# Performance work log

Measured on AMD Instinct MI355X. Metric: run time of the kernel, lower is better.

The kernel has to match this reference:

```python
import jax, jax.numpy as jnp
import numpy as np

NUM_CLASSES = 80
PRE_NMS_K = 400    # pre_nms_points / max_output_size_per_class
MAX_BOXES = 200    # max_total_size
NMS_THRESH = 0.6
SCORE_THRESH = 0.0  # iou_thresh in YoloLayer, used as score threshold/mask
SCALE_XY = (1.2, 1.1, 1.05)  # levels 3,4,5
STRIDES = (8.0, 16.0, 32.0)  # 2**level


def setup_inputs() -> dict:
    key = jax.random.key(0)
    k3, k4, k5 = jax.random.split(key, 3)
    B, C5 = 8, 3 * (NUM_CLASSES + 5)
    p3 = jax.random.normal(k3, (B, 64, 64, C5), dtype=jnp.float32)
    p4 = jax.random.normal(k4, (B, 32, 32, C5), dtype=jnp.float32)
    p5 = jax.random.normal(k5, (B, 16, 16, C5), dtype=jnp.float32)
    a3 = jnp.array([[12., 16.], [19., 36.], [40., 28.]], jnp.float32)
    a4 = jnp.array([[36., 75.], [76., 55.], [72., 146.]], jnp.float32)
    a5 = jnp.array([[142., 110.], [192., 243.], [459., 401.]], jnp.float32)
    return {"p3": p3, "p4": p4, "p5": p5, "a3": a3, "a4": a4, "a5": a5}


def _decode_level(p, anchors, stride, scale_xy):
    # p: [B,H,W,A*(C+5)] raw head output; 'original' box decode (sigmoid xy, exp wh)
    B, H, W, _ = p.shape
    A = anchors.shape[0]
    d = p.reshape(B, H, W, A, NUM_CLASSES + 5)
    txy, twh, tobj, tcls = d[..., :2], d[..., 2:4], d[..., 4:5], d[..., 5:]
    gx, gy = jnp.meshgrid(jnp.arange(W, dtype=p.dtype), jnp.arange(H, dtype=p.dtype))
    grid = jnp.stack([gx, gy], -1)[None, :, :, None, :]          # [1,H,W,1,2] (x,y)
    sxy = jnp.asarray(scale_xy, p.dtype)
    xy = (jax.nn.sigmoid(txy) * sxy - 0.5 * (sxy - 1.0) + grid) / jnp.array([W, H], p.dtype)
    wh = jnp.exp(twh) * anchors[None, None, None] / jnp.array([W * stride, H * stride], p.dtype)
    x1y1 = xy - 0.5 * wh
    x2y2 = xy + 0.5 * wh
    boxes = jnp.stack([x1y1[..., 1], x1y1[..., 0], x2y2[..., 1], x2y2[..., 0]], -1)  # yxyx
    obj = jax.nn.sigmoid(tobj)
    cls = jax.nn.sigmoid(tcls) * obj
    N = H * W * A
    return boxes.reshape(B, N, 4), cls.reshape(B, N, NUM_CLASSES), obj.reshape(B, N)


def _pairwise_iou(b):
    # b: [K,4] yxyx in [0,1]
    area = (b[:, 2] - b[:, 0]) * (b[:, 3] - b[:, 1])
    tl = jnp.maximum(b[:, None, :2], b[None, :, :2])
    br = jnp.minimum(b[:, None, 2:], b[None, :, 2:])
    wh = jnp.maximum(br - tl, 0.0)
    inter = wh[..., 0] * wh[..., 1]
    union = area[:, None] + area[None, :] - inter
    return inter / jnp.maximum(union, 1e-9)


def _greedy_nms_scores(boxes, scores):
    # boxes/scores already sorted by score descending; returns scores with suppressed -> 0
    K = scores.shape[0]
    overlap = _pairwise_iou(boxes) > NMS_THRESH
    idx = jnp.arange(K)

    def body(i, keep):
        sup = overlap[i] & (idx > i) & keep[i]
        return keep & ~sup

    keep = jax.lax.fori_loop(0, K, body, jnp.ones((K,), bool))
    return jnp.where(keep & (scores > SCORE_THRESH), scores, 0.0)


def _detections_per_image(boxes, cls_scores):
    # boxes [N,4], cls_scores [N,C] -> combined per-class NMS, top MAX_BOXES overall
    boxes = jnp.clip(boxes, 0.0, 1.0)  # combined NMS clips boxes by default

    def per_class(scores_c):
        vals, idx = jax.lax.top_k(scores_c, PRE_NMS_K)
        b = boxes[idx]
        return _greedy_nms_scores(b, vals), b

    kept_scores, kept_boxes = jax.vmap(per_class)(cls_scores.T)  # [C,K], [C,K,4]
    flat_s = kept_scores.reshape(-1)
    flat_b = kept_boxes.reshape(-1, 4)
    cls_ids = jnp.repeat(jnp.arange(NUM_CLASSES), PRE_NMS_K)
    top_s, top_i = jax.lax.top_k(flat_s, MAX_BOXES)
    top_b = flat_b[top_i]
    top_c = cls_ids[top_i].astype(jnp.float32)
    valid = top_s > 0.0
    top_b = jnp.where(valid[:, None], top_b, 0.0)
    top_c = jnp.where(valid, top_c, 0.0)
    num = jnp.sum(valid.astype(jnp.int32))
    return top_b, top_s, top_c, num


def _forward(p3, p4, p5, a3, a4, a5):
    boxes, cls_scores, obj_scores = [], [], []
    for (p, a), stride, sxy in zip(((p3, a3), (p4, a4), (p5, a5)), STRIDES, SCALE_XY):
        b, c, o = _decode_level(p, a, stride, sxy)
        boxes.append(b); cls_scores.append(c); obj_scores.append(o)
    boxes = jnp.concatenate(boxes, 1)            # [B,N,4]
    cls_scores = jnp.concatenate(cls_scores, 1)  # [B,N,C]
    obj_scores = jnp.concatenate(obj_scores, 1)  # [B,N]
    obj_mask = (obj_scores > SCORE_THRESH).astype(boxes.dtype)
    cls_mask = (cls_scores > SCORE_THRESH).astype(boxes.dtype)
    cls_scores = cls_scores * obj_mask[..., None] * cls_mask
    return jax.vmap(_detections_per_image)(boxes, cls_scores)


def reference(p3, p4, p5, a3, a4, a5):
    bbox, confidence, classes, num_detections = _forward(p3, p4, p5, a3, a4, a5)
    return bbox, confidence, classes, num_detections
```

## Files before the change

### kernel.cpp

```cpp
#include <hip/hip_runtime.h>
#include <math.h>

#define NCLS 80
#define PRE_K 400
#define MAX_BOXES 200
#define KEEP_CAP 200
#define N_TOT 16128
#define M_FIN (NCLS * KEEP_CAP)
#define NMS_T 0.6f
#define NTHR 512
#define CAP 512

typedef unsigned long long u64;
typedef unsigned int u32;
typedef unsigned short u16;

__device__ __forceinline__ float sigf(float x) { return 1.0f / (1.0f + expf(-x)); }

__device__ __forceinline__ float score_f32(int idx, int b, int c,
    const float* __restrict__ p3, const float* __restrict__ p4, const float* __restrict__ p5)
{
    const float* base; int W, n;
    if (idx < 12288)      { base = p3; W = 64; n = idx; }
    else if (idx < 15360) { base = p4; W = 32; n = idx - 12288; }
    else                  { base = p5; W = 16; n = idx - 15360; }
    int a = n % 3, hw = n / 3, w = hw % W, h = hw / W;
    const float* rec = base + (((b * W + h) * W + w) * 255 + a * 85);
    return sigf(rec[5 + c]) * sigf(rec[4]);
}

__device__ __forceinline__ void hist_agg(u32* hist, u32 d, bool valid, int lane)
{
    u64 act = __ballot(valid);
    while (act) {
        int ldr = __ffsll((unsigned long long)act) - 1;
        u32 dl = __shfl(d, ldr, 64);
        u64 m = __ballot(valid && d == dl);
        if (lane == ldr) atomicAdd(&hist[dl], (u32)__popcll(m));
        act &= ~m;
    }
}

__device__ __forceinline__ void digit_select(const u32* hist, int need,
                                             u32* sh_dg, u32* sh_S1, u32* sh_T, int tid)
{
    if (tid < 64) {
        const int lane = tid;
        u32 h0 = hist[4 * lane + 0], h1 = hist[4 * lane + 1];
        u32 h2 = hist[4 * lane + 2], h3 = hist[4 * lane + 3];
        u32 loc = h0 + h1 + h2 + h3;
        u32 s = loc;
#pragma unroll
        for (int off = 1; off < 64; off <<= 1) {
            u32 t = __shfl_down(s, off, 64);
            if (lane + off < 64) s += t;
        }
        u32 after = s - loc;
        u32 S3 = h3 + after, S2 = h2 + S3, S1v = h1 + S2, S0 = h0 + S1v;
        u32 Sarr[5] = { S0, S1v, S2, S3, after };
#pragma unroll
        for (int k = 0; k < 4; ++k) {
            if ((int)Sarr[k] >= need && need > (int)Sarr[k + 1]) {
                *sh_dg = (u32)(4 * lane + k);
                *sh_S1 = Sarr[k + 1];
                *sh_T  = Sarr[k] - Sarr[k + 1];
            }
        }
    }
    __syncthreads();
}

__device__ __forceinline__ void sort512(u64* cand, int tid)
{
    u64 v = cand[tid];
#pragma unroll
    for (int k2 = 2; k2 <= 64; k2 <<= 1) {
#pragma unroll
        for (int j = k2 >> 1; j > 0; j >>= 1) {
            u64 p = __shfl_xor(v, j, 64);
            bool takeMax = ((tid & k2) == 0) ^ ((tid & j) != 0);
            v = takeMax ? (v >= p ? v : p) : (v <= p ? v : p);
        }
    }
    for (int k2 = 128; k2 <= CAP; k2 <<= 1) {
        for (int j = k2 >> 1; j >= 64; j >>= 1) {
            __syncthreads();
            cand[tid] = v;
            __syncthreads();
            u64 p = cand[tid ^ j];
            bool takeMax = ((tid & k2) == 0) ^ ((tid & j) != 0);
            v = takeMax ? (v >= p ? v : p) : (v <= p ? v : p);
        }
#pragma unroll
        for (int j = 32; j > 0; j >>= 1) {
            u64 p = __shfl_xor(v, j, 64);
            bool takeMax = ((tid & k2) == 0) ^ ((tid & j) != 0);
            v = takeMax ? (v >= p ? v : p) : (v <= p ? v : p);
        }
    }
    __syncthreads();
    cand[tid] = v;
    __syncthreads();
}

__global__ __launch_bounds__(256) void decode_kernel(
    const float* __restrict__ p3, const float* __restrict__ p4, const float* __restrict__ p5,
    const float* __restrict__ a3, const float* __restrict__ a4, const float* __restrict__ a5,
    u16* __restrict__ scores16, float* __restrict__ boxes)
{
    const int blk = blockIdx.x;
    const int b = blk & 7;
    const int n = ((blk >> 3) << 8) + threadIdx.x;

    const float* base; const float* anc; int logw, nn; float sx;
    if (n < 12288)      { base = p3; anc = a3; logw = 6; nn = n;         sx = 1.2f;  }
    else if (n < 15360) { base = p4; anc = a4; logw = 5; nn = n - 12288; sx = 1.1f;  }
    else                { base = p5; anc = a5; logw = 4; nn = n - 15360; sx = 1.05f; }
    const int W = 1 << logw;
    const int a = nn % 3; const int hw = nn / 3;
    const int w = hw & (W - 1); const int h = hw >> logw;
    const float winv = 1.0f / (float)W;
    const float* rec = base + ((size_t)((b * W + h) * W + w) * 255 + a * 85);

    float tx = rec[0], ty = rec[1], tw = rec[2], th = rec[3], to = rec[4];
    float sobj = sigf(to);
    float cx = (sigf(tx) * sx - 0.5f * (sx - 1.0f) + (float)w) * winv;
    float cy = (sigf(ty) * sx - 0.5f * (sx - 1.0f) + (float)h) * winv;
    float bw = expf(tw) * anc[a * 2 + 0] * (1.0f / 512.0f);
    float bh = expf(th) * anc[a * 2 + 1] * (1.0f / 512.0f);
    float x1 = cx - 0.5f * bw, x2 = cx + 0.5f * bw;
    float y1 = cy - 0.5f * bh, y2 = cy + 0.5f * bh;
    y1 = fminf(fmaxf(y1, 0.f), 1.f); x1 = fminf(fmaxf(x1, 0.f), 1.f);
    y2 = fminf(fmaxf(y2, 0.f), 1.f); x2 = fminf(fmaxf(x2, 0.f), 1.f);
    float4 bb; bb.x = y1; bb.y = x1; bb.z = y2; bb.w = x2;
    ((float4*)boxes)[b * N_TOT + n] = bb;

    u16* sb = scores16 + (long)b * NCLS * N_TOT + n;
#pragma unroll 8
    for (int cc = 0; cc < NCLS; ++cc)
        sb[(long)cc * N_TOT] = (u16)(__float_as_uint(sigf(rec[5 + cc]) * sobj) >> 16);
}

__global__ __launch_bounds__(NTHR, 4) void topk_nms_fused(
    const u16* __restrict__ scores16, const float* __restrict__ boxes,
    const float* __restrict__ p3, const float* __restrict__ p4, const float* __restrict__ p5,
    float* __restrict__ ksc, float* __restrict__ kbox)
{
    __shared__ alignas(16) u16 skey[N_TOT];
    __shared__ alignas(16) u64 cand[CAP];
    __shared__ u32 hist[260];
    __shared__ u32 sh_dg, sh_S1, sh_T;
    __shared__ int sh_gcnt;
    __shared__ alignas(16) float boxbuf[5 * 448];
    __shared__ alignas(16) u64 diagbuf[64];
    __shared__ u32 keepb[16];
    __shared__ u64 sh_keptM;
    __shared__ int wpre14[14];
    __shared__ int sh_ncnt;

    float* by1 = boxbuf;
    float* bx1 = boxbuf + 448;
    float* by2 = boxbuf + 896;
    float* bx2 = boxbuf + 1344;
    float* bar = boxbuf + 1792;

    const int tid = threadIdx.x;
    const int wv = tid >> 6;
    const int lane = tid & 63;
    const int b = blockIdx.x & 7;
    const int c = blockIdx.x >> 3;

    const u16* keys16g = scores16 + (long)(b * NCLS + c) * N_TOT;
    const uint4* k4g = (const uint4*)keys16g;
    const uint4* k4 = (const uint4*)skey;
    const int N8 = N_TOT >> 3;

    if (tid < 260) hist[tid] = 0u;
    if (tid == 0) sh_gcnt = 0;
    __syncthreads();
#pragma unroll
    for (int it = 0; it < 4; ++it) {
        int i4 = tid + it * NTHR;
        bool v = i4 < N8;
        u32 e0 = 0, e1 = 0, e2 = 0, e3 = 0, e4 = 0, e5 = 0, e6 = 0, e7 = 0;
        if (v) {
            uint4 kk = k4g[i4];
            ((uint4*)skey)[i4] = kk;
            e0 = kk.x & 0xffffu; e1 = kk.x >> 16; e2 = kk.y & 0xffffu; e3 = kk.y >> 16;
            e4 = kk.z & 0xffffu; e5 = kk.z >> 16; e6 = kk.w & 0xffffu; e7 = kk.w >> 16;
        }
        hist_agg(hist, e0 >> 8, v, lane); hist_agg(hist, e1 >> 8, v, lane);
        hist_agg(hist, e2 >> 8, v, lane); hist_agg(hist, e3 >> 8, v, lane);
        hist_agg(hist, e4 >> 8, v, lane); hist_agg(hist, e5 >> 8, v, lane);
        hist_agg(hist, e6 >> 8, v, lane); hist_agg(hist, e7 >> 8, v, lane);
    }
    __syncthreads();

    int need = PRE_K;
    digit_select(hist, need, &sh_dg, &sh_S1, &sh_T, tid);
    u32 thr = sh_dg; need -= (int)sh_S1;
    int C = (PRE_K - need) + (int)sh_T;
    int lvl = 1;

    if (C > CAP) {
        if (tid < 256) hist[tid] = 0u;
        __syncthreads();
#pragma unroll
        for (int it = 0; it < 4; ++it) {
            int i4 = tid + it * NTHR;
            if (i4 < N8) {
                uint4 kk = k4[i4];
                u32 e[8] = { kk.x & 0xffffu, kk.x >> 16, kk.y & 0xffffu, kk.y >> 16,
                             kk.z & 0xffffu, kk.z >> 16, kk.w & 0xffffu, kk.w >> 16 };
#pragma unroll
                for (int q = 0; q < 8; ++q)
                    if ((e[q] >> 8) == thr) atomicAdd(&hist[e[q] & 255u], 1u);
            }
        }
        __syncthreads();
        digit_select(hist, need, &sh_dg, &sh_S1, &sh_T, tid);
        thr = (thr << 8) | sh_dg; need -= (int)sh_S1;
        C = (PRE_K - need) + (int)sh_T;
        lvl = 2;
    }

    if (C > CAP) {
        u32 t16 = thr;
        if (tid < 256) hist[tid] = 0u;
        __syncthreads();
        for (int i = tid; i < N_TOT; i += NTHR) {
            if (skey[i] == (u16)t16) {
                u32 kb = __float_as_uint(score_f32(i, b, c, p3, p4, p5));
                atomicAdd(&hist[(kb >> 8) & 255u], 1u);
            }
        }
        __syncthreads();
        digit_select(hist, need, &sh_dg, &sh_S1, &sh_T, tid);
        thr = (thr << 8) | sh_dg; need -= (int)sh_S1;
        C = (PRE_K - need) + (int)sh_T;
        lvl = 3;
    }

    if (C > CAP) {
        u32 t16 = thr >> 8;
        if (tid < 256) hist[tid] = 0u;
        __syncthreads();
        for (int i = tid; i < N_TOT; i += NTHR) {
            if (skey[i] == (u16)t16) {
                u32 kb = __float_as_uint(score_f32(i, b, c, p3, p4, p5));
                if ((kb >> 8) == thr) atomicAdd(&hist[kb & 255u], 1u);
            }
        }
        __syncthreads();
        digit_select(hist, need, &sh_dg, &sh_S1, &sh_T, tid);
        thr = (thr << 8) | sh_dg; need -= (int)sh_S1;
        C = (PRE_K - need) + (int)sh_T;
        lvl = 4;
    }

    if (lvl <= 2) {
#pragma unroll
        for (int it = 0; it < 4; ++it) {
            int i4 = tid + it * NTHR;
            if (i4 < N8) {
                uint4 kk = k4[i4];
                int i0 = i4 << 3;
                u32 e[8] = { kk.x & 0xffffu, kk.x >> 16, kk.y & 0xffffu, kk.y >> 16,
                             kk.z & 0xffffu, kk.z >> 16, kk.w & 0xffffu, kk.w >> 16 };
#pragma unroll
                for (int q = 0; q < 8; ++q) {
                    bool take = (lvl == 1) ? ((e[q] >> 8) >= thr) : (e[q] >= thr);
                    if (take) {
                        int p = atomicAdd(&sh_gcnt, 1);
                        int i = i0 + q;
                        u32 kb = __float_as_uint(score_f32(i, b, c, p3, p4, p5));
                        cand[p] = ((u64)kb << 32) | (u32)(0xFFFFFFFFu - (u32)i);
                    }
                }
            }
        }
        __syncthreads();
        for (int t = C + tid; t < CAP; t += NTHR) cand[t] = 0ull;
    } else if (C <= CAP) {
        u32 t16 = (lvl == 3) ? (thr >> 8) : (thr >> 16);
        for (int i = tid; i < N_TOT; i += NTHR) {
            u32 k = skey[i];
            bool take = false;
            u32 kb = 0;
            if (k > t16) { take = true; kb = __float_as_uint(score_f32(i, b, c, p3, p4, p5)); }
            else if (k == t16) {
                kb = __float_as_uint(score_f32(i, b, c, p3, p4, p5));
                take = (lvl == 3) ? ((kb >> 8) >= thr) : (kb >= thr);
            }
            if (take) {
                int p = atomicAdd(&sh_gcnt, 1);
                cand[p] = ((u64)kb << 32) | (u32)(0xFFFFFFFFu - (u32)i);
            }
        }
        __syncthreads();
        for (int t = C + tid; t < CAP; t += NTHR) cand[t] = 0ull;
    } else {
        u32 t16 = thr >> 16;
        for (int i = tid; i < N_TOT; i += NTHR) {
            u32 k = skey[i];
            if (k < t16) continue;
            u32 kb = __float_as_uint(score_f32(i, b, c, p3, p4, p5));
            if (kb > thr) {
                int p = atomicAdd(&sh_gcnt, 1);
                cand[p] = ((u64)kb << 32) | (u32)(0xFFFFFFFFu - (u32)i);
            }
        }
        __syncthreads();
        const int G = sh_gcnt;
        u32* scr = (u32*)boxbuf;
        int lo = tid * 32; if (lo > N_TOT) lo = N_TOT;
        int hi = lo + 32;  if (hi > N_TOT) hi = N_TOT;
        int lc = 0;
        for (int i = lo; i < hi; ++i)
            if (skey[i] == (u16)t16 &&
                __float_as_uint(score_f32(i, b, c, p3, p4, p5)) == thr) ++lc;
        u32* sc_cur = scr; u32* sc_oth = scr + 512;
        sc_cur[tid] = (u32)lc;
        __syncthreads();
        for (int off = 1; off < NTHR; off <<= 1) {
            sc_oth[tid] = sc_cur[tid] + ((tid >= off) ? sc_cur[tid - off] : 0u);
            __syncthreads();
            u32* tmp = sc_cur; sc_cur = sc_oth; sc_oth = tmp;
        }
        int r = (int)sc_cur[tid] - lc;
        for (int i = lo; i < hi; ++i) {
            if (skey[i] == (u16)t16 &&
                __float_as_uint(score_f32(i, b, c, p3, p4, p5)) == thr) {
                if (r < need) cand[G + r] = ((u64)thr << 32) | (u32)(0xFFFFFFFFu - (u32)i);
                ++r;
            }
        }
        __syncthreads();
        for (int t = PRE_K + tid; t < CAP; t += NTHR) cand[t] = 0ull;
    }
    __syncthreads();

    sort512(cand, tid);

    const float4* btab = (const float4*)boxes;
    for (int t = tid; t < 448; t += NTHR) {
        float y1 = 0.f, x1 = 0.f, y2 = 0.f, x2 = 0.f;
        if (t < PRE_K) {
            u64 key = cand[t];
            if ((key >> 32) != 0ull) {
                int idx = (int)(0xFFFFFFFFu - (u32)(key & 0xFFFFFFFFull));
                float4 bb = btab[b * N_TOT + idx];
                y1 = bb.x; x1 = bb.y; y2 = bb.z; x2 = bb.w;
            }
        }
        by1[t] = y1; bx1[t] = x1; by2[t] = y2; bx2[t] = x2;
        bar[t] = (y2 - y1) * (x2 - x1);
    }
    if (tid < 16) keepb[tid] = (tid < 12) ? 0xFFFFFFFFu : ((tid == 12) ? 0xFFFFu : 0u);
    __syncthreads();

    for (int ch = 0; ch < 7; ++ch) {
        const int rbase = ch << 6;
        const float ry1 = by1[rbase + lane], rx1v = bx1[rbase + lane];
        const float ry2 = by2[rbase + lane], rx2v = bx2[rbase + lane];
        const float ra  = bar[rbase + lane];

#pragma unroll
        for (int q = 0; q < 8; ++q) {
            const int jl = wv * 8 + q;
            const int jj = rbase + jl;
            u64 m = 0ull;
            if (jj < PRE_K && ((keepb[jj >> 5] >> (jj & 31)) & 1u)) {
                float cy1 = by1[jj], cx1 = bx1[jj], cy2 = by2[jj], cx2 = bx2[jj], ca = bar[jj];
                float ty = fmaxf(ry1, cy1), tx = fmaxf(rx1v, cx1);
                float byv = fminf(ry2, cy2), rxv = fminf(rx2v, cx2);
                float inter = fmaxf(byv - ty, 0.f) * fmaxf(rxv - tx, 0.f);
                float uni = ra + ca - inter;
                bool o = (lane < jl) && ((inter / fmaxf(uni, 1e-9f)) > NMS_T);
                m = __ballot(o);
            }
            if (lane == 0) diagbuf[jl] = m;
        }
        __syncthreads();

        if (tid < 64) {
            u64 dg = diagbuf[lane];
            int ri = rbase + lane;
            int alive = (ri < PRE_K) ? (int)((keepb[ri >> 5] >> (ri & 31)) & 1u) : 0;
            u64 M = __ballot(alive != 0);
            for (int i = 0; i < 64; ++i) {
                if ((M >> i) & 1ull) {
                    int kill = (int)((dg >> i) & 1ull);
                    alive &= ~kill;
                    M = __ballot(alive != 0);
                }
            }
            if (lane == 0) {
                sh_keptM = M;
                keepb[2 * ch]     = (u32)(M & 0xFFFFFFFFull);
                keepb[2 * ch + 1] = (u32)(M >> 32);
            }
        }
        __syncthreads();

        {
            const u64 keptM = sh_keptM;
            if (keptM != 0ull) {
                for (int jj = rbase + 64 + wv; jj < PRE_K; jj += 8) {
                    if ((keepb[jj >> 5] >> (jj & 31)) & 1u) {
                        float cy1 = by1[jj], cx1 = bx1[jj], cy2 = by2[jj], cx2 = bx2[jj], ca = bar[jj];
                        float ty = fmaxf(ry1, cy1), tx = fmaxf(rx1v, cx1);
                        float byv = fminf(ry2, cy2), rxv = fminf(rx2v, cx2);
                        float inter = fmaxf(byv - ty, 0.f) * fmaxf(rxv - tx, 0.f);
                        float uni = ra + ca - inter;
                        bool o = (inter / fmaxf(uni, 1e-9f)) > NMS_T;
                        u64 m = __ballot(o);
                        if ((m & keptM) != 0ull && lane == 0)
                            atomicAnd(&keepb[jj >> 5], ~(1u << (jj & 31)));
                    }
                }
            }
        }
        __syncthreads();
    }

    if (tid == 0) {
        int acc = 0;
        for (int w = 0; w < 14; ++w) { wpre14[w] = acc; acc += __popc(keepb[w]); }
        sh_ncnt = acc < KEEP_CAP ? acc : KEEP_CAP;
    }
    __syncthreads();

    const int blk_out = b * NCLS + c;
    float* osc = ksc + (long)blk_out * KEEP_CAP;
    float* obx = kbox + (long)blk_out * KEEP_CAP * 4;
    for (int t = tid; t < PRE_K; t += NTHR) {
        u32 kw = keepb[t >> 5];
        if ((kw >> (t & 31)) & 1u) {
            int pos = wpre14[t >> 5] + __popc(kw & ((1u << (t & 31)) - 1u));
            if (pos < KEEP_CAP) {
                osc[pos] = __uint_as_float((u32)(cand[t] >> 32));
                obx[pos * 4 + 0] = by1[t]; obx[pos * 4 + 1] = bx1[t];
                obx[pos * 4 + 2] = by2[t]; obx[pos * 4 + 3] = bx2[t];
            }
        }
    }
    for (int t = sh_ncnt + tid; t < KEEP_CAP; t += NTHR) {
        osc[t] = 0.0f;
        obx[t * 4 + 0] = 0.f; obx[t * 4 + 1] = 0.f;
        obx[t * 4 + 2] = 0.f; obx[t * 4 + 3] = 0.f;
    }
}

__device__ __forceinline__ void radix_topk_sort_f32(
    const u32* __restrict__ keys, int n, int K,
    u64* cand, u32* hist, u32* scr,
    u32* sh_dg, u32* sh_S1, u32* sh_T, int* sh_gcnt, int tid)
{
    int need = K;
    digit_select(hist, need, sh_dg, sh_S1, sh_T, tid);
    u32 thr = *sh_dg; need -= (int)*sh_S1;
    int C = (K - need) + (int)*sh_T;
    int eshift = 24;

    const uint4* k4 = (const uint4*)keys;
    const int n4 = n >> 2;
    const int nIter = (n4 + NTHR - 1) / NTHR;

    for (int shift = 16; shift >= 0 && C > CAP; shift -= 8) {
        if (tid < 256) hist[tid] = 0u;
        __syncthreads();
        for (int it = 0; it < nIter; ++it) {
            int i4 = tid + it * NTHR;
            if (i4 < n4) {
                uint4 kk = k4[i4];
                if ((kk.x >> (shift + 8)) == thr) atomicAdd(&hist[(kk.x >> shift) & 255u], 1u);
                if ((kk.y >> (shift + 8)) == thr) atomicAdd(&hist[(kk.y >> shift) & 255u], 1u);
                if ((kk.z >> (shift + 8)) == thr) atomicAdd(&hist[(kk.z >> shift) & 255u], 1u);
                if ((kk.w >> (shift + 8)) == thr) atomicAdd(&hist[(kk.w >> shift) & 255u], 1u);
            }
        }
        __syncthreads();
        digit_select(hist, need, sh_dg, sh_S1, sh_T, tid);
        thr = (thr << 8) | *sh_dg; need -= (int)*sh_S1;
        C = (K - need) + (int)*sh_T;
        eshift = shift;
    }

    if (C <= CAP) {
        for (int it = 0; it < nIter; ++it) {
            int i4 = tid + it * NTHR;
            if (i4 < n4) {
                uint4 kk = k4[i4];
                int i0 = i4 << 2;
                if ((kk.x >> eshift) >= thr) { int p = atomicAdd(sh_gcnt, 1); cand[p] = ((u64)kk.x << 32) | (u32)(0xFFFFFFFFu - (u32)(i0 + 0)); }
                if ((kk.y >> eshift) >= thr) { int p = atomicAdd(sh_gcnt, 1); cand[p] = ((u64)kk.y << 32) | (u32)(0xFFFFFFFFu - (u32)(i0 + 1)); }
                if ((kk.z >> eshift) >= thr) { int p = atomicAdd(sh_gcnt, 1); cand[p] = ((u64)kk.z << 32) | (u32)(0xFFFFFFFFu - (u32)(i0 + 2)); }
                if ((kk.w >> eshift) >= thr) { int p = atomicAdd(sh_gcnt, 1); cand[p] = ((u64)kk.w << 32) | (u32)(0xFFFFFFFFu - (u32)(i0 + 3)); }
            }
        }
        __syncthreads();
        for (int t = C + tid; t < CAP; t += NTHR) cand[t] = 0ull;
    } else {
        for (int i = tid; i < n; i += NTHR) {
            u32 k = keys[i];
            if (k > thr) {
                int p = atomicAdd(sh_gcnt, 1);
                cand[p] = ((u64)k << 32) | (u32)(0xFFFFFFFFu - (u32)i);
            }
        }
        __syncthreads();
        const int G = *sh_gcnt;
        int lo = tid * 32; if (lo > n) lo = n;
        int hi = lo + 32;  if (hi > n) hi = n;
        int lc = 0;
        for (int i = lo; i < hi; ++i) if (keys[i] == thr) ++lc;
        u32* sc_cur = scr; u32* sc_oth = scr + 512;
        sc_cur[tid] = (u32)lc;
        __syncthreads();
        for (int off = 1; off < NTHR; off <<= 1) {
            sc_oth[tid] = sc_cur[tid] + ((tid >= off) ? sc_cur[tid - off] : 0u);
            __syncthreads();
            u32* tmp = sc_cur; sc_cur = sc_oth; sc_oth = tmp;
        }
        int r = (int)sc_cur[tid] - lc;
        for (int i = lo; i < hi; ++i) {
            if (keys[i] == thr) {
                if (r < need) cand[G + r] = ((u64)thr << 32) | (u32)(0xFFFFFFFFu - (u32)i);
                ++r;
            }
        }
        __syncthreads();
        for (int t = K + tid; t < CAP; t += NTHR) cand[t] = 0ull;
    }
    __syncthreads();
    sort512(cand, tid);
}

__global__ __launch_bounds__(NTHR) void final_topk_kernel(
    const float* __restrict__ ksc, const float* __restrict__ kbox,
    float* __restrict__ out)
{
    __shared__ alignas(16) u64 cand[CAP];
    __shared__ u32 hist[260];
    __shared__ u32 scr[1024];
    __shared__ u32 sh_dg, sh_S1, sh_T;
    __shared__ int sh_gcnt;

    const int tid = threadIdx.x;
    const int lane = tid & 63;
    const int b = blockIdx.x;
    const u32* keys = (const u32*)(ksc + (long)b * M_FIN);

    if (tid < 260) hist[tid] = 0u;
    if (tid == 0) sh_gcnt = 0;
    __syncthreads();
    const uint4* k4 = (const uint4*)keys;
#pragma unroll
    for (int it = 0; it < 8; ++it) {
        int i4 = tid + it * NTHR;
        bool v = i4 < (M_FIN >> 2);
        u32 d0 = 0, d1 = 0, d2 = 0, d3 = 0;
        if (v) {
            uint4 kk = k4[i4];
            d0 = kk.x >> 24; d1 = kk.y >> 24; d2 = kk.z >> 24; d3 = kk.w >> 24;
        }
        hist_agg(hist, d0, v, lane);
        hist_agg(hist, d1, v, lane);
        hist_agg(hist, d2, v, lane);
        hist_agg(hist, d3, v, lane);
    }
    __syncthreads();

    radix_topk_sort_f32(keys, M_FIN, MAX_BOXES, cand, hist, scr,
                        &sh_dg, &sh_S1, &sh_T, &sh_gcnt, tid);

    float* obb = out;
    float* ocf = out + 8 * MAX_BOXES * 4;
    float* ocl = ocf + 8 * MAX_BOXES;
    float* onm = ocl + 8 * MAX_BOXES;

    float s = 0.f;
    if (tid < MAX_BOXES) {
        u64 key = cand[tid];
        s = __uint_as_float((u32)(key >> 32));
        float y1 = 0.f, x1 = 0.f, y2 = 0.f, x2 = 0.f, cid = 0.f;
        if (s > 0.0f) {
            int i = (int)(0xFFFFFFFFu - (u32)(key & 0xFFFFFFFFull));
            int cc = i / KEEP_CAP, j = i % KEEP_CAP;
            const float* bb = kbox + (((long)b * NCLS + cc) * KEEP_CAP + j) * 4;
            y1 = bb[0]; x1 = bb[1]; y2 = bb[2]; x2 = bb[3];
            cid = (float)cc;
        }
        long o = (long)b * MAX_BOXES + tid;
        obb[o * 4 + 0] = y1; obb[o * 4 + 1] = x1; obb[o * 4 + 2] = y2; obb[o * 4 + 3] = x2;
        ocf[o] = s; ocl[o] = cid;
    }
    int cnt = __syncthreads_count(tid < MAX_BOXES && s > 0.0f);
    if (tid == 0) onm[b] = (float)cnt;
}

extern "C" void kernel_launch(void* const* d_in, const int* in_sizes, int n_in,
                              void* d_out, int out_size, void* d_ws, size_t ws_size,
                              hipStream_t stream) {
    const float* p3 = (const float*)d_in[0];
    const float* p4 = (const float*)d_in[1];
    const float* p5 = (const float*)d_in[2];
    const float* a3 = (const float*)d_in[3];
    const float* a4 = (const float*)d_in[4];
    const float* a5 = (const float*)d_in[5];
    float* out = (float*)d_out;

    const size_t s16_bytes  = (size_t)8 * NCLS * N_TOT * 2;
    const size_t box_bytes  = (size_t)8 * N_TOT * 16;
    const size_t ksc_bytes  = (size_t)8 * NCLS * KEEP_CAP * 4;

    u16*   scores16 = (u16*)d_ws;
    float* boxes    = (float*)((char*)d_ws + s16_bytes);
    float* ksc      = (float*)((char*)d_ws + s16_bytes + box_bytes);
    float* kbox     = (float*)((char*)d_ws + s16_bytes + box_bytes + ksc_bytes);

    decode_kernel<<<504, 256, 0, stream>>>(p3, p4, p5, a3, a4, a5, scores16, boxes);
    topk_nms_fused<<<8 * NCLS, NTHR, 0, stream>>>(scores16, boxes, p3, p4, p5, ksc, kbox);
    final_topk_kernel<<<8, NTHR, 0, stream>>>(ksc, kbox, out);
}
```

Before: 169.0 us.

## Widen top-k/NMS blocks to 1024 threads and hold score keys in registers

The fused top-k/NMS kernel now runs 1024 threads per block. It drops the 32KB shared-memory copy of the per-class 16-bit keys: each thread keeps its two uint4 key chunks in registers, and the rarer deeper-radix paths re-read the keys from global memory. The bitonic sort gains a variant that masks off threads above 512, and the NMS wave loop and scan are rescaled to 16 waves. This is meant to cut LDS pressure and raise parallelism per block. In exchange it adds register pressure under 1024-thread launch bounds and makes the fallback paths read global memory.

```diff
diff --git a/kernel.cpp b/kernel.cpp
--- a/kernel.cpp
+++ b/kernel.cpp
@@ -8,7 +8,9 @@
 #define N_TOT 16128
 #define M_FIN (NCLS * KEEP_CAP)
 #define NMS_T 0.6f
-#define NTHR 512
+#define NTHR 1024
+#define NWAVE (NTHR / 64)
+#define FTHR 512
 #define CAP 512
 
 typedef unsigned long long u64;
@@ -100,6 +102,46 @@
     }
     __syncthreads();
     cand[tid] = v;
+    __syncthreads();
+}
+
+__device__ __forceinline__ void sort512_wide(u64* cand, int tid)
+{
+    u64 v = 0ull;
+    if (tid < 512) {
+        v = cand[tid];
+#pragma unroll
+        for (int k2 = 2; k2 <= 64; k2 <<= 1) {
+#pragma unroll
+            for (int j = k2 >> 1; j > 0; j >>= 1) {
+                u64 p = __shfl_xor(v, j, 64);
+                bool takeMax = ((tid & k2) == 0) ^ ((tid & j) != 0);
+                v = takeMax ? (v >= p ? v : p) : (v <= p ? v : p);
+            }
+        }
+    }
+    for (int k2 = 128; k2 <= CAP; k2 <<= 1) {
+        for (int j = k2 >> 1; j >= 64; j >>= 1) {
+            __syncthreads();
+            if (tid < 512) cand[tid] = v;
+            __syncthreads();
+            if (tid < 512) {
+                u64 p = cand[tid ^ j];
+                bool takeMax = ((tid & k2) == 0) ^ ((tid & j) != 0);
+                v = takeMax ? (v >= p ? v : p) : (v <= p ? v : p);
+            }
+        }
+        if (tid < 512) {
+#pragma unroll
+            for (int j = 32; j > 0; j >>= 1) {
+                u64 p = __shfl_xor(v, j, 64);
+                bool takeMax = ((tid & k2) == 0) ^ ((tid & j) != 0);
+                v = takeMax ? (v >= p ? v : p) : (v <= p ? v : p);
+            }
+        }
+    }
+    __syncthreads();
+    if (tid < 512) cand[tid] = v;
     __syncthreads();
 }
 
@@ -141,12 +183,11 @@
         sb[(long)cc * N_TOT] = (u16)(__float_as_uint(sigf(rec[5 + cc]) * sobj) >> 16);
 }
 
-__global__ __launch_bounds__(NTHR, 4) void topk_nms_fused(
+__global__ __launch_bounds__(NTHR, 2) void topk_nms_fused(
     const u16* __restrict__ scores16, const float* __restrict__ boxes,
     const float* __restrict__ p3, const float* __restrict__ p4, const float* __restrict__ p5,
     float* __restrict__ ksc, float* __restrict__ kbox)
 {
-    __shared__ alignas(16) u16 skey[N_TOT];
     __shared__ alignas(16) u64 cand[CAP];
     __shared__ u32 hist[260];
     __shared__ u32 sh_dg, sh_S1, sh_T;
@@ -172,28 +213,24 @@
 
     const u16* keys16g = scores16 + (long)(b * NCLS + c) * N_TOT;
     const uint4* k4g = (const uint4*)keys16g;
-    const uint4* k4 = (const uint4*)skey;
     const int N8 = N_TOT >> 3;
 
     if (tid < 260) hist[tid] = 0u;
     if (tid == 0) sh_gcnt = 0;
-    __syncthreads();
-#pragma unroll
-    for (int it = 0; it < 4; ++it) {
-        int i4 = tid + it * NTHR;
-        bool v = i4 < N8;
-        u32 e0 = 0, e1 = 0, e2 = 0, e3 = 0, e4 = 0, e5 = 0, e6 = 0, e7 = 0;
-        if (v) {
-            uint4 kk = k4g[i4];
-            ((uint4*)skey)[i4] = kk;
-            e0 = kk.x & 0xffffu; e1 = kk.x >> 16; e2 = kk.y & 0xffffu; e3 = kk.y >> 16;
-            e4 = kk.z & 0xffffu; e5 = kk.z >> 16; e6 = kk.w & 0xffffu; e7 = kk.w >> 16;
-        }
-        hist_agg(hist, e0 >> 8, v, lane); hist_agg(hist, e1 >> 8, v, lane);
-        hist_agg(hist, e2 >> 8, v, lane); hist_agg(hist, e3 >> 8, v, lane);
-        hist_agg(hist, e4 >> 8, v, lane); hist_agg(hist, e5 >> 8, v, lane);
-        hist_agg(hist, e6 >> 8, v, lane); hist_agg(hist, e7 >> 8, v, lane);
-    }
+    const uint4 kA = k4g[tid];
+    const bool vB = (tid + NTHR) < N8;
+    uint4 kB; kB.x = 0u; kB.y = 0u; kB.z = 0u; kB.w = 0u;
+    if (vB) kB = k4g[tid + NTHR];
+    u32 eA[8] = { kA.x & 0xffffu, kA.x >> 16, kA.y & 0xffffu, kA.y >> 16,
+                  kA.z & 0xffffu, kA.z >> 16, kA.w & 0xffffu, kA.w >> 16 };
+    u32 eB[8] = { kB.x & 0xffffu, kB.x >> 16, kB.y & 0xffffu, kB.y >> 16,
+                  kB.z & 0xffffu, kB.z >> 16, kB.w & 0xffffu, kB.w >> 16 };
+    __syncthreads();
+
+#pragma unroll
+    for (int q = 0; q < 8; ++q) hist_agg(hist, eA[q] >> 8, true, lane);
+#pragma unroll
+    for (int q = 0; q < 8; ++q) hist_agg(hist, eB[q] >> 8, vB, lane);
     __syncthreads();
 
     int need = PRE_K;
@@ -206,16 +243,12 @@
         if (tid < 256) hist[tid] = 0u;
         __syncthreads();
 #pragma unroll
-        for (int it = 0; it < 4; ++it) {
-            int i4 = tid + it * NTHR;
-            if (i4 < N8) {
-                uint4 kk = k4[i4];
-                u32 e[8] = { kk.x & 0xffffu, kk.x >> 16, kk.y & 0xffffu, kk.y >> 16,
-                             kk.z & 0xffffu, kk.z >> 16, kk.w & 0xffffu, kk.w >> 16 };
-#pragma unroll
-                for (int q = 0; q < 8; ++q)
-                    if ((e[q] >> 8) == thr) atomicAdd(&hist[e[q] & 255u], 1u);
-            }
+        for (int q = 0; q < 8; ++q)
+            if ((eA[q] >> 8) == thr) atomicAdd(&hist[eA[q] & 255u], 1u);
+        if (vB) {
+#pragma unroll
+            for (int q = 0; q < 8; ++q)
+                if ((eB[q] >> 8) == thr) atomicAdd(&hist[eB[q] & 255u], 1u);
         }
         __syncthreads();
         digit_select(hist, need, &sh_dg, &sh_S1, &sh_T, tid);
@@ -229,7 +262,7 @@
         if (tid < 256) hist[tid] = 0u;
         __syncthreads();
         for (int i = tid; i < N_TOT; i += NTHR) {
-            if (skey[i] == (u16)t16) {
+            if (keys16g[i] == (u16)t16) {
                 u32 kb = __float_as_uint(score_f32(i, b, c, p3, p4, p5));
                 atomicAdd(&hist[(kb >> 8) & 255u], 1u);
             }
@@ -246,7 +279,7 @@
         if (tid < 256) hist[tid] = 0u;
         __syncthreads();
         for (int i = tid; i < N_TOT; i += NTHR) {
-            if (skey[i] == (u16)t16) {
+            if (keys16g[i] == (u16)t16) {
                 u32 kb = __float_as_uint(score_f32(i, b, c, p3, p4, p5));
                 if ((kb >> 8) == thr) atomicAdd(&hist[kb & 255u], 1u);
             }
@@ -260,22 +293,24 @@
 
     if (lvl <= 2) {
 #pragma unroll
-        for (int it = 0; it < 4; ++it) {
-            int i4 = tid + it * NTHR;
-            if (i4 < N8) {
-                uint4 kk = k4[i4];
-                int i0 = i4 << 3;
-                u32 e[8] = { kk.x & 0xffffu, kk.x >> 16, kk.y & 0xffffu, kk.y >> 16,
-                             kk.z & 0xffffu, kk.z >> 16, kk.w & 0xffffu, kk.w >> 16 };
-#pragma unroll
-                for (int q = 0; q < 8; ++q) {
-                    bool take = (lvl == 1) ? ((e[q] >> 8) >= thr) : (e[q] >= thr);
-                    if (take) {
-                        int p = atomicAdd(&sh_gcnt, 1);
-                        int i = i0 + q;
-                        u32 kb = __float_as_uint(score_f32(i, b, c, p3, p4, p5));
-                        cand[p] = ((u64)kb << 32) | (u32)(0xFFFFFFFFu - (u32)i);
-                    }
+        for (int q = 0; q < 8; ++q) {
+            bool take = (lvl == 1) ? ((eA[q] >> 8) >= thr) : (eA[q] >= thr);
+            if (take) {
+                int p = atomicAdd(&sh_gcnt, 1);
+                int i = (tid << 3) + q;
+                u32 kb = __float_as_uint(score_f32(i, b, c, p3, p4, p5));
+                cand[p] = ((u64)kb << 32) | (u32)(0xFFFFFFFFu - (u32)i);
+            }
+        }
+        if (vB) {
+#pragma unroll
+            for (int q = 0; q < 8; ++q) {
+                bool take = (lvl == 1) ? ((eB[q] >> 8) >= thr) : (eB[q] >= thr);
+                if (take) {
+                    int p = atomicAdd(&sh_gcnt, 1);
+                    int i = ((tid + NTHR) << 3) + q;
+                    u32 kb = __float_as_uint(score_f32(i, b, c, p3, p4, p5));
+                    cand[p] = ((u64)kb << 32) | (u32)(0xFFFFFFFFu - (u32)i);
                 }
             }
         }
@@ -284,7 +319,7 @@
     } else if (C <= CAP) {
         u32 t16 = (lvl == 3) ? (thr >> 8) : (thr >> 16);
         for (int i = tid; i < N_TOT; i += NTHR) {
-            u32 k = skey[i];
+            u32 k = keys16g[i];
             bool take = false;
             u32 kb = 0;
             if (k > t16) { take = true; kb = __float_as_uint(score_f32(i, b, c, p3, p4, p5)); }
@@ -302,7 +337,7 @@
     } else {
         u32 t16 = thr >> 16;
         for (int i = tid; i < N_TOT; i += NTHR) {
-            u32 k = skey[i];
+            u32 k = keys16g[i];
             if (k < t16) continue;
             u32 kb = __float_as_uint(score_f32(i, b, c, p3, p4, p5));
             if (kb > thr) {
@@ -313,13 +348,13 @@
         __syncthreads();
         const int G = sh_gcnt;
         u32* scr = (u32*)boxbuf;
-        int lo = tid * 32; if (lo > N_TOT) lo = N_TOT;
-        int hi = lo + 32;  if (hi > N_TOT) hi = N_TOT;
+        int lo = tid * 16; if (lo > N_TOT) lo = N_TOT;
+        int hi = lo + 16;  if (hi > N_TOT) hi = N_TOT;
         int lc = 0;
         for (int i = lo; i < hi; ++i)
-            if (skey[i] == (u16)t16 &&
+            if (keys16g[i] == (u16)t16 &&
                 __float_as_uint(score_f32(i, b, c, p3, p4, p5)) == thr) ++lc;
-        u32* sc_cur = scr; u32* sc_oth = scr + 512;
+        u32* sc_cur = scr; u32* sc_oth = scr + NTHR;
         sc_cur[tid] = (u32)lc;
         __syncthreads();
         for (int off = 1; off < NTHR; off <<= 1) {
@@ -329,7 +364,7 @@
         }
         int r = (int)sc_cur[tid] - lc;
         for (int i = lo; i < hi; ++i) {
-            if (skey[i] == (u16)t16 &&
+            if (keys16g[i] == (u16)t16 &&
                 __float_as_uint(score_f32(i, b, c, p3, p4, p5)) == thr) {
                 if (r < need) cand[G + r] = ((u64)thr << 32) | (u32)(0xFFFFFFFFu - (u32)i);
                 ++r;
@@ -340,7 +375,7 @@
     }
     __syncthreads();
 
-    sort512(cand, tid);
+    sort512_wide(cand, tid);
 
     const float4* btab = (const float4*)boxes;
     for (int t = tid; t < 448; t += NTHR) {
@@ -366,8 +401,8 @@
         const float ra  = bar[rbase + lane];
 
 #pragma unroll
-        for (int q = 0; q < 8; ++q) {
-            const int jl = wv * 8 + q;
+        for (int q = 0; q < 4; ++q) {
+            const int jl = wv * 4 + q;
             const int jj = rbase + jl;
             u64 m = 0ull;
             if (jj < PRE_K && ((keepb[jj >> 5] >> (jj & 31)) & 1u)) {
@@ -406,7 +441,7 @@
         {
             const u64 keptM = sh_keptM;
             if (keptM != 0ull) {
-                for (int jj = rbase + 64 + wv; jj < PRE_K; jj += 8) {
+                for (int jj = rbase + 64 + wv; jj < PRE_K; jj += NWAVE) {
                     if ((keepb[jj >> 5] >> (jj & 31)) & 1u) {
                         float cy1 = by1[jj], cx1 = bx1[jj], cy2 = by2[jj], cx2 = bx2[jj], ca = bar[jj];
                         float ty = fmaxf(ry1, cy1), tx = fmaxf(rx1v, cx1);
@@ -465,13 +500,13 @@
 
     const uint4* k4 = (const uint4*)keys;
     const int n4 = n >> 2;
-    const int nIter = (n4 + NTHR - 1) / NTHR;
+    const int nIter = (n4 + FTHR - 1) / FTHR;
 
     for (int shift = 16; shift >= 0 && C > CAP; shift -= 8) {
         if (tid < 256) hist[tid] = 0u;
         __syncthreads();
         for (int it = 0; it < nIter; ++it) {
-            int i4 = tid + it * NTHR;
+            int i4 = tid + it * FTHR;
             if (i4 < n4) {
                 uint4 kk = k4[i4];
                 if ((kk.x >> (shift + 8)) == thr) atomicAdd(&hist[(kk.x >> shift) & 255u], 1u);
@@ -489,7 +524,7 @@
 
     if (C <= CAP) {
         for (int it = 0; it < nIter; ++it) {
-            int i4 = tid + it * NTHR;
+            int i4 = tid + it * FTHR;
             if (i4 < n4) {
                 uint4 kk = k4[i4];
                 int i0 = i4 << 2;
@@ -500,9 +535,9 @@
             }
         }
         __syncthreads();
-        for (int t = C + tid; t < CAP; t += NTHR) cand[t] = 0ull;
+        for (int t = C + tid; t < CAP; t += FTHR) cand[t] = 0ull;
     } else {
-        for (int i = tid; i < n; i += NTHR) {
+        for (int i = tid; i < n; i += FTHR) {
             u32 k = keys[i];
             if (k > thr) {
                 int p = atomicAdd(sh_gcnt, 1);
@@ -518,7 +553,7 @@
         u32* sc_cur = scr; u32* sc_oth = scr + 512;
         sc_cur[tid] = (u32)lc;
         __syncthreads();
-        for (int off = 1; off < NTHR; off <<= 1) {
+        for (int off = 1; off < FTHR; off <<= 1) {
             sc_oth[tid] = sc_cur[tid] + ((tid >= off) ? sc_cur[tid - off] : 0u);
             __syncthreads();
             u32* tmp = sc_cur; sc_cur = sc_oth; sc_oth = tmp;
@@ -531,13 +566,13 @@
             }
         }
         __syncthreads();
-        for (int t = K + tid; t < CAP; t += NTHR) cand[t] = 0ull;
+        for (int t = K + tid; t < CAP; t += FTHR) cand[t] = 0ull;
     }
     __syncthreads();
     sort512(cand, tid);
 }
 
-__global__ __launch_bounds__(NTHR) void final_topk_kernel(
+__global__ __launch_bounds__(FTHR) void final_topk_kernel(
     const float* __restrict__ ksc, const float* __restrict__ kbox,
     float* __restrict__ out)
 {
@@ -558,7 +593,7 @@
     const uint4* k4 = (const uint4*)keys;
 #pragma unroll
     for (int it = 0; it < 8; ++it) {
-        int i4 = tid + it * NTHR;
+        int i4 = tid + it * FTHR;
         bool v = i4 < (M_FIN >> 2);
         u32 d0 = 0, d1 = 0, d2 = 0, d3 = 0;
         if (v) {
@@ -622,5 +657,5 @@
 
     decode_kernel<<<504, 256, 0, stream>>>(p3, p4, p5, a3, a4, a5, scores16, boxes);
     topk_nms_fused<<<8 * NCLS, NTHR, 0, stream>>>(scores16, boxes, p3, p4, p5, ksc, kbox);
-    final_topk_kernel<<<8, NTHR, 0, stream>>>(ksc, kbox, out);
-}
+    final_topk_kernel<<<8, FTHR, 0, stream>>>(ksc, kbox, out);
+}
```

New measurement: 179.4 us. +6.2%, slower.

## Drop shared key copy in top-k kernel, raise occupancy, use shuffle-based NMS diagonal

Applied to the files above, without the earlier changes.

Removes the 32KB shared-memory copy of the per-class 16-bit score keys. Later passes re-read the keys from global memory, which lets the launch-bounds hint ask for 8 blocks per CU instead of 4. The intra-chunk NMS diagonal resolution is reworked: the previous loop issued a ballot per alive row, and the new one does a shuffle plus a mask update per row on a 64-bit kept mask. Re-reading keys from global (L2) adds memory traffic in the refinement passes, and a tighter register budget may spill.

```diff
diff --git a/kernel.cpp b/kernel.cpp
--- a/kernel.cpp
+++ b/kernel.cpp
@@ -9,6 +9,8 @@
 #define M_FIN (NCLS * KEEP_CAP)
 #define NMS_T 0.6f
 #define NTHR 512
+#define NWAVE (NTHR / 64)
+#define FTHR 512
 #define CAP 512
 
 typedef unsigned long long u64;
@@ -141,12 +143,11 @@
         sb[(long)cc * N_TOT] = (u16)(__float_as_uint(sigf(rec[5 + cc]) * sobj) >> 16);
 }
 
-__global__ __launch_bounds__(NTHR, 4) void topk_nms_fused(
+__global__ __launch_bounds__(NTHR, 8) void topk_nms_fused(
     const u16* __restrict__ scores16, const float* __restrict__ boxes,
     const float* __restrict__ p3, const float* __restrict__ p4, const float* __restrict__ p5,
     float* __restrict__ ksc, float* __restrict__ kbox)
 {
-    __shared__ alignas(16) u16 skey[N_TOT];
     __shared__ alignas(16) u64 cand[CAP];
     __shared__ u32 hist[260];
     __shared__ u32 sh_dg, sh_S1, sh_T;
@@ -172,7 +173,6 @@
 
     const u16* keys16g = scores16 + (long)(b * NCLS + c) * N_TOT;
     const uint4* k4g = (const uint4*)keys16g;
-    const uint4* k4 = (const uint4*)skey;
     const int N8 = N_TOT >> 3;
 
     if (tid < 260) hist[tid] = 0u;
@@ -182,17 +182,14 @@
     for (int it = 0; it < 4; ++it) {
         int i4 = tid + it * NTHR;
         bool v = i4 < N8;
-        u32 e0 = 0, e1 = 0, e2 = 0, e3 = 0, e4 = 0, e5 = 0, e6 = 0, e7 = 0;
+        u32 e[8] = { 0,0,0,0,0,0,0,0 };
         if (v) {
             uint4 kk = k4g[i4];
-            ((uint4*)skey)[i4] = kk;
-            e0 = kk.x & 0xffffu; e1 = kk.x >> 16; e2 = kk.y & 0xffffu; e3 = kk.y >> 16;
-            e4 = kk.z & 0xffffu; e5 = kk.z >> 16; e6 = kk.w & 0xffffu; e7 = kk.w >> 16;
-        }
-        hist_agg(hist, e0 >> 8, v, lane); hist_agg(hist, e1 >> 8, v, lane);
-        hist_agg(hist, e2 >> 8, v, lane); hist_agg(hist, e3 >> 8, v, lane);
-        hist_agg(hist, e4 >> 8, v, lane); hist_agg(hist, e5 >> 8, v, lane);
-        hist_agg(hist, e6 >> 8, v, lane); hist_agg(hist, e7 >> 8, v, lane);
+            e[0] = kk.x & 0xffffu; e[1] = kk.x >> 16; e[2] = kk.y & 0xffffu; e[3] = kk.y >> 16;
+            e[4] = kk.z & 0xffffu; e[5] = kk.z >> 16; e[6] = kk.w & 0xffffu; e[7] = kk.w >> 16;
+        }
+#pragma unroll
+        for (int q = 0; q < 8; ++q) hist_agg(hist, e[q] >> 8, v, lane);
     }
     __syncthreads();
 
@@ -209,7 +206,7 @@
         for (int it = 0; it < 4; ++it) {
             int i4 = tid + it * NTHR;
             if (i4 < N8) {
-                uint4 kk = k4[i4];
+                uint4 kk = k4g[i4];
                 u32 e[8] = { kk.x & 0xffffu, kk.x >> 16, kk.y & 0xffffu, kk.y >> 16,
                              kk.z & 0xffffu, kk.z >> 16, kk.w & 0xffffu, kk.w >> 16 };
 #pragma unroll
@@ -229,7 +226,7 @@
         if (tid < 256) hist[tid] = 0u;
         __syncthreads();
         for (int i = tid; i < N_TOT; i += NTHR) {
-            if (skey[i] == (u16)t16) {
+            if (keys16g[i] == (u16)t16) {
                 u32 kb = __float_as_uint(score_f32(i, b, c, p3, p4, p5));
                 atomicAdd(&hist[(kb >> 8) & 255u], 1u);
             }
@@ -246,7 +243,7 @@
         if (tid < 256) hist[tid] = 0u;
         __syncthreads();
         for (int i = tid; i < N_TOT; i += NTHR) {
-            if (skey[i] == (u16)t16) {
+            if (keys16g[i] == (u16)t16) {
                 u32 kb = __float_as_uint(score_f32(i, b, c, p3, p4, p5));
                 if ((kb >> 8) == thr) atomicAdd(&hist[kb & 255u], 1u);
             }
@@ -263,7 +260,7 @@
         for (int it = 0; it < 4; ++it) {
             int i4 = tid + it * NTHR;
             if (i4 < N8) {
-                uint4 kk = k4[i4];
+                uint4 kk = k4g[i4];
                 int i0 = i4 << 3;
                 u32 e[8] = { kk.x & 0xffffu, kk.x >> 16, kk.y & 0xffffu, kk.y >> 16,
                              kk.z & 0xffffu, kk.z >> 16, kk.w & 0xffffu, kk.w >> 16 };
@@ -284,7 +281,7 @@
     } else if (C <= CAP) {
         u32 t16 = (lvl == 3) ? (thr >> 8) : (thr >> 16);
         for (int i = tid; i < N_TOT; i += NTHR) {
-            u32 k = skey[i];
+            u32 k = keys16g[i];
             bool take = false;
             u32 kb = 0;
             if (k > t16) { take = true; kb = __float_as_uint(score_f32(i, b, c, p3, p4, p5)); }
@@ -302,7 +299,7 @@
     } else {
         u32 t16 = thr >> 16;
         for (int i = tid; i < N_TOT; i += NTHR) {
-            u32 k = skey[i];
+            u32 k = keys16g[i];
             if (k < t16) continue;
             u32 kb = __float_as_uint(score_f32(i, b, c, p3, p4, p5));
             if (kb > thr) {
@@ -317,9 +314,9 @@
         int hi = lo + 32;  if (hi > N_TOT) hi = N_TOT;
         int lc = 0;
         for (int i = lo; i < hi; ++i)
-            if (skey[i] == (u16)t16 &&
+            if (keys16g[i] == (u16)t16 &&
                 __float_as_uint(score_f32(i, b, c, p3, p4, p5)) == thr) ++lc;
-        u32* sc_cur = scr; u32* sc_oth = scr + 512;
+        u32* sc_cur = scr; u32* sc_oth = scr + NTHR;
         sc_cur[tid] = (u32)lc;
         __syncthreads();
         for (int off = 1; off < NTHR; off <<= 1) {
@@ -329,7 +326,7 @@
         }
         int r = (int)sc_cur[tid] - lc;
         for (int i = lo; i < hi; ++i) {
-            if (skey[i] == (u16)t16 &&
+            if (keys16g[i] == (u16)t16 &&
                 __float_as_uint(score_f32(i, b, c, p3, p4, p5)) == thr) {
                 if (r < need) cand[G + r] = ((u64)thr << 32) | (u32)(0xFFFFFFFFu - (u32)i);
                 ++r;
@@ -367,38 +364,36 @@
 
 #pragma unroll
         for (int q = 0; q < 8; ++q) {
-            const int jl = wv * 8 + q;
-            const int jj = rbase + jl;
+            const int rl = wv * 8 + q;
+            const int rr = rbase + rl;
             u64 m = 0ull;
-            if (jj < PRE_K && ((keepb[jj >> 5] >> (jj & 31)) & 1u)) {
-                float cy1 = by1[jj], cx1 = bx1[jj], cy2 = by2[jj], cx2 = bx2[jj], ca = bar[jj];
-                float ty = fmaxf(ry1, cy1), tx = fmaxf(rx1v, cx1);
-                float byv = fminf(ry2, cy2), rxv = fminf(rx2v, cx2);
+            bool rowAlive = (rr < PRE_K) && ((keepb[rr >> 5] >> (rr & 31)) & 1u);
+            if (rowAlive) {
+                float qy1 = by1[rr], qx1 = bx1[rr], qy2 = by2[rr], qx2 = bx2[rr], qa = bar[rr];
+                float ty = fmaxf(qy1, ry1), tx = fmaxf(qx1, rx1v);
+                float byv = fminf(qy2, ry2), rxv = fminf(qx2, rx2v);
                 float inter = fmaxf(byv - ty, 0.f) * fmaxf(rxv - tx, 0.f);
-                float uni = ra + ca - inter;
-                bool o = (lane < jl) && ((inter / fmaxf(uni, 1e-9f)) > NMS_T);
+                float uni = qa + ra - inter;
+                bool o = (lane > rl) && ((inter / fmaxf(uni, 1e-9f)) > NMS_T);
                 m = __ballot(o);
             }
-            if (lane == 0) diagbuf[jl] = m;
+            if (lane == 0) diagbuf[rl] = m;
         }
         __syncthreads();
 
         if (tid < 64) {
-            u64 dg = diagbuf[lane];
-            int ri = rbase + lane;
-            int alive = (ri < PRE_K) ? (int)((keepb[ri >> 5] >> (ri & 31)) & 1u) : 0;
-            u64 M = __ballot(alive != 0);
+            u64 dgrow = diagbuf[lane];
+            u64 kept = ((u64)keepb[2 * ch + 1] << 32) | (u64)keepb[2 * ch];
+#pragma unroll 16
             for (int i = 0; i < 64; ++i) {
-                if ((M >> i) & 1ull) {
-                    int kill = (int)((dg >> i) & 1ull);
-                    alive &= ~kill;
-                    M = __ballot(alive != 0);
-                }
+                u64 dgi = __shfl(dgrow, i);
+                u64 msk = 0ull - ((kept >> i) & 1ull);
+                kept &= ~(dgi & msk);
             }
             if (lane == 0) {
-                sh_keptM = M;
-                keepb[2 * ch]     = (u32)(M & 0xFFFFFFFFull);
-                keepb[2 * ch + 1] = (u32)(M >> 32);
+                sh_keptM = kept;
+                keepb[2 * ch]     = (u32)(kept & 0xFFFFFFFFull);
+                keepb[2 * ch + 1] = (u32)(kept >> 32);
             }
         }
         __syncthreads();
@@ -406,7 +401,7 @@
         {
             const u64 keptM = sh_keptM;
             if (keptM != 0ull) {
-                for (int jj = rbase + 64 + wv; jj < PRE_K; jj += 8) {
+                for (int jj = rbase + 64 + wv; jj < PRE_K; jj += NWAVE) {
                     if ((keepb[jj >> 5] >> (jj & 31)) & 1u) {
                         float cy1 = by1[jj], cx1 = bx1[jj], cy2 = by2[jj], cx2 = bx2[jj], ca = bar[jj];
                         float ty = fmaxf(ry1, cy1), tx = fmaxf(rx1v, cx1);
@@ -465,13 +460,13 @@
 
     const uint4* k4 = (const uint4*)keys;
     const int n4 = n >> 2;
-    const int nIter = (n4 + NTHR - 1) / NTHR;
+    const int nIter = (n4 + FTHR - 1) / FTHR;
 
     for (int shift = 16; shift >= 0 && C > CAP; shift -= 8) {
         if (tid < 256) hist[tid] = 0u;
         __syncthreads();
         for (int it = 0; it < nIter; ++it) {
-            int i4 = tid + it * NTHR;
+            int i4 = tid + it * FTHR;
             if (i4 < n4) {
                 uint4 kk = k4[i4];
                 if ((kk.x >> (shift + 8)) == thr) atomicAdd(&hist[(kk.x >> shift) & 255u], 1u);
@@ -489,7 +484,7 @@
 
     if (C <= CAP) {
         for (int it = 0; it < nIter; ++it) {
-            int i4 = tid + it * NTHR;
+            int i4 = tid + it * FTHR;
             if (i4 < n4) {
                 uint4 kk = k4[i4];
                 int i0 = i4 << 2;
@@ -500,9 +495,9 @@
             }
         }
         __syncthreads();
-        for (int t = C + tid; t < CAP; t += NTHR) cand[t] = 0ull;
+        for (int t = C + tid; t < CAP; t += FTHR) cand[t] = 0ull;
     } else {
-        for (int i = tid; i < n; i += NTHR) {
+        for (int i = tid; i < n; i += FTHR) {
             u32 k = keys[i];
             if (k > thr) {
                 int p = atomicAdd(sh_gcnt, 1);
@@ -518,7 +513,7 @@
         u32* sc_cur = scr; u32* sc_oth = scr + 512;
         sc_cur[tid] = (u32)lc;
         __syncthreads();
-        for (int off = 1; off < NTHR; off <<= 1) {
+        for (int off = 1; off < FTHR; off <<= 1) {
             sc_oth[tid] = sc_cur[tid] + ((tid >= off) ? sc_cur[tid - off] : 0u);
             __syncthreads();
             u32* tmp = sc_cur; sc_cur = sc_oth; sc_oth = tmp;
@@ -531,13 +526,13 @@
             }
         }
         __syncthreads();
-        for (int t = K + tid; t < CAP; t += NTHR) cand[t] = 0ull;
+        for (int t = K + tid; t < CAP; t += FTHR) cand[t] = 0ull;
     }
     __syncthreads();
     sort512(cand, tid);
 }
 
-__global__ __launch_bounds__(NTHR) void final_topk_kernel(
+__global__ __launch_bounds__(FTHR) void final_topk_kernel(
     const float* __restrict__ ksc, const float* __restrict__ kbox,
     float* __restrict__ out)
 {
@@ -558,7 +553,7 @@
     const uint4* k4 = (const uint4*)keys;
 #pragma unroll
     for (int it = 0; it < 8; ++it) {
-        int i4 = tid + it * NTHR;
+        int i4 = tid + it * FTHR;
         bool v = i4 < (M_FIN >> 2);
         u32 d0 = 0, d1 = 0, d2 = 0, d3 = 0;
         if (v) {
@@ -622,5 +617,5 @@
 
     decode_kernel<<<504, 256, 0, stream>>>(p3, p4, p5, a3, a4, a5, scores16, boxes);
     topk_nms_fused<<<8 * NCLS, NTHR, 0, stream>>>(scores16, boxes, p3, p4, p5, ksc, kbox);
-    final_topk_kernel<<<8, NTHR, 0, stream>>>(ksc, kbox, out);
-}
+    final_topk_kernel<<<8, FTHR, 0, stream>>>(ksc, kbox, out);
+}
```

Measured after the change: 185.7 us. 1.1x slower.
